# Optimization experiments

Measured on AMD Instinct MI355X. Metric: run time of the kernel, lower is better.

## Reference

```python
import math
import jax, jax.numpy as jnp
import numpy as np

N_HEAD = 8


def setup_inputs() -> dict:
    key = jax.random.key(0)
    ks = jax.random.split(key, 9)
    B, S, D = 4, 2048, 512
    s = 1.0 / math.sqrt(D)
    return {
        "x": jax.random.normal(ks[0], (B, S, D), jnp.float32),
        "Wq": jax.random.normal(ks[1], (D, D), jnp.float32) * s,
        "bq": jax.random.normal(ks[2], (D,), jnp.float32) * s,
        "Wk": jax.random.normal(ks[3], (D, D), jnp.float32) * s,
        "bk": jax.random.normal(ks[4], (D,), jnp.float32) * s,
        "Wv": jax.random.normal(ks[5], (D, D), jnp.float32) * s,
        "bv": jax.random.normal(ks[6], (D,), jnp.float32) * s,
        "Wo": jax.random.normal(ks[7], (D, D), jnp.float32) * s,
        "bo": jax.random.normal(ks[8], (D,), jnp.float32) * s,
    }


def reference(x, Wq, bq, Wk, bk, Wv, bv, Wo, bo):
    B, S, D = x.shape
    H = N_HEAD
    hd = D // H
    # projections -> [B, H, S, hd]
    def split_heads(y):
        return y.reshape(B, S, H, hd).transpose(0, 2, 1, 3)
    q = split_heads(x @ Wq + bq)
    k = split_heads(x @ Wk + bk)
    v = split_heads(x @ Wv + bv)
    scale = 1.0 / math.sqrt(hd)
    scores = jnp.einsum("bhqd,bhkd->bhqk", q, k) * scale  # [B,H,S,S]
    attn = jax.nn.softmax(scores, axis=-1)
    ctx = jnp.einsum("bhqk,bhkd->bhqd", attn, v)  # [B,H,S,hd]
    ctx = ctx.transpose(0, 2, 1, 3).reshape(B, S, D)
    out = ctx @ Wo + bo
    avg_attn = attn.mean(axis=1)  # [B,S,S]
    return out, avg_attn
```

## Files before the change

kernel.cpp:

```cpp
#include <hip/hip_runtime.h>

typedef __bf16 bf16;
typedef __bf16 bf16x8 __attribute__((ext_vector_type(8)));
typedef float  f32x4  __attribute__((ext_vector_type(4)));
typedef float  f32x16 __attribute__((ext_vector_type(16)));

#define MFMA16(a,b,c) __builtin_amdgcn_mfma_f32_16x16x32_bf16((a),(b),(c),0,0,0)
#define MFMA32(a,b,c) __builtin_amdgcn_mfma_f32_32x32x16_bf16((a),(b),(c),0,0,0)

#define BATCH 4
#define SEQ   2048
#define DIM   512
#define NH    8
#define HD    64
#define QSCALE 0.18033688f

__device__ __forceinline__ bf16x8 ldsfrag(const bf16* t, int row, int kc, int quad){
    int unit = ((kc << 2) + quad) ^ (row & 7);
    return *(const bf16x8*)(t + row * 64 + unit * 8);
}
__device__ __forceinline__ bf16x8 ldsfrag32(const bf16* t, int row, int unit){
    return *(const bf16x8*)(t + row * 64 + ((unit ^ (row & 7)) << 3));
}

__device__ __forceinline__ void stage64x64(const bf16* src, long rowStride, bf16* dst, int tid){
#pragma unroll
    for (int rnd = 0; rnd < 2; ++rnd){
        int sid = tid + rnd * 256;
        int row = sid >> 3, s = sid & 7;
        bf16x8 val = *(const bf16x8*)(src + (long)row * rowStride + s * 8);
        *(bf16x8*)(dst + row * 64 + ((s ^ (row & 7)) << 3)) = val;
    }
}

__global__ __launch_bounds__(256) void cvt_x(const float* __restrict__ x, bf16* __restrict__ xb){
    int i = blockIdx.x * 256 + threadIdx.x;
    float4 f = ((const float4*)x)[i];
    bf16* o = xb + 4 * (long)i;
    o[0] = (bf16)f.x; o[1] = (bf16)f.y; o[2] = (bf16)f.z; o[3] = (bf16)f.w;
}

__global__ __launch_bounds__(256) void cvt_wt(const float* __restrict__ Wq, const float* __restrict__ Wk,
                                              const float* __restrict__ Wv, const float* __restrict__ Wo,
                                              bf16* __restrict__ WTb){
    int z = blockIdx.z;
    const float* W = (z == 0) ? Wq : (z == 1) ? Wk : (z == 2) ? Wv : Wo;
    bf16* WT = WTb + (long)z * DIM * DIM;
    __shared__ float lt[32 * 33];
    int t = threadIdx.x, r0 = t >> 5, c = t & 31;
    int k0 = blockIdx.x * 32, n0 = blockIdx.y * 32;
#pragma unroll
    for (int i = 0; i < 4; ++i){
        int row = r0 + i * 8;
        lt[row * 33 + c] = W[(long)(k0 + row) * DIM + n0 + c];
    }
    __syncthreads();
#pragma unroll
    for (int i = 0; i < 4; ++i){
        int nr = r0 + i * 8;
        WT[(long)(n0 + nr) * DIM + k0 + c] = (bf16)lt[c * 33 + nr];
    }
}

__global__ __launch_bounds__(256) void gemm_qkv(const bf16* __restrict__ X, const bf16* __restrict__ WTb,
                                                const float* __restrict__ bq, const float* __restrict__ bk,
                                                const float* __restrict__ bv, bf16* __restrict__ outb){
    __shared__ __align__(16) bf16 lA[128 * 64];
    __shared__ __align__(16) bf16 lB[128 * 64];
    int z = blockIdx.z;
    const bf16* WT = WTb + (long)z * DIM * DIM;
    const float* bias = (z == 0) ? bq : (z == 1) ? bk : bv;
    float qs = (z == 0) ? QSCALE : 1.0f;
    bf16* out = outb + (long)z * BATCH * SEQ * DIM;
    int tid = threadIdx.x, lane = tid & 63, w = tid >> 6;
    int wm = w >> 1, wn = w & 1;
    int m0 = blockIdx.y * 128, n0 = blockIdx.x * 128;
    int r16 = lane & 15, quad = lane >> 4;
    f32x4 zz = {0.f, 0.f, 0.f, 0.f};
    f32x4 acc[4][4];
#pragma unroll
    for (int a = 0; a < 4; ++a)
#pragma unroll
        for (int b2 = 0; b2 < 4; ++b2) acc[a][b2] = zz;

    for (int k0 = 0; k0 < DIM; k0 += 64){
        __syncthreads();
#pragma unroll
        for (int rnd = 0; rnd < 4; ++rnd){
            int sid = tid + rnd * 256;
            int row = sid >> 3, s = sid & 7;
            *(bf16x8*)(lA + row * 64 + ((s ^ (row & 7)) << 3)) =
                *(const bf16x8*)(X + (long)(m0 + row) * DIM + k0 + s * 8);
            *(bf16x8*)(lB + row * 64 + ((s ^ (row & 7)) << 3)) =
                *(const bf16x8*)(WT + (long)(n0 + row) * DIM + k0 + s * 8);
        }
        __syncthreads();
#pragma unroll
        for (int kc = 0; kc < 2; ++kc){
            bf16x8 aF[4], bF[4];
#pragma unroll
            for (int i = 0; i < 4; ++i){
                aF[i] = ldsfrag(lA, wm * 64 + i * 16 + r16, kc, quad);
                bF[i] = ldsfrag(lB, wn * 64 + i * 16 + r16, kc, quad);
            }
#pragma unroll
            for (int rb = 0; rb < 4; ++rb)
#pragma unroll
                for (int nb = 0; nb < 4; ++nb)
                    acc[rb][nb] = MFMA16(aF[rb], bF[nb], acc[rb][nb]);
        }
    }
#pragma unroll
    for (int nb = 0; nb < 4; ++nb){
        int col = n0 + wn * 64 + nb * 16 + r16;
        float bv_ = bias[col];
        int hh = col >> 6, d = col & 63;
#pragma unroll
        for (int rb = 0; rb < 4; ++rb)
#pragma unroll
            for (int r = 0; r < 4; ++r){
                int row = m0 + wm * 64 + rb * 16 + quad * 4 + r;
                int bb = row >> 11, s = row & 2047;
                out[((long)(bb * NH + hh) * SEQ + s) * HD + d] = (bf16)((acc[rb][nb][r] + bv_) * qs);
            }
    }
}

__global__ __launch_bounds__(256) void vtrans(const bf16* __restrict__ v, bf16* __restrict__ vT){
    __shared__ bf16 lt[64 * 72];
    int tid = threadIdx.x;
    int s0 = blockIdx.x * 64;
    int bh = blockIdx.z * NH + blockIdx.y;
#pragma unroll
    for (int rnd = 0; rnd < 2; ++rnd){
        int sid = tid + rnd * 256;
        int row = sid >> 3, sg = sid & 7;
        *(bf16x8*)(lt + row * 72 + sg * 8) =
            *(const bf16x8*)(v + ((long)bh * SEQ + s0 + row) * HD + sg * 8);
    }
    __syncthreads();
#pragma unroll
    for (int rnd = 0; rnd < 2; ++rnd){
        int sid = tid + rnd * 256;
        int d = sid >> 3, sg = sid & 7;
        bf16x8 o;
#pragma unroll
        for (int j = 0; j < 8; ++j) o[j] = lt[(sg * 8 + j) * 72 + d];
        *(bf16x8*)(vT + ((long)bh * HD + d) * SEQ + s0 + sg * 8) = o;
    }
}

__global__ __launch_bounds__(256) void attn_flash(const bf16* __restrict__ q, const bf16* __restrict__ k,
                                                  const bf16* __restrict__ vT, bf16* __restrict__ ctx,
                                                  float* __restrict__ llv_g){
    __shared__ __align__(16) bf16 lQ[128 * 64];
    __shared__ __align__(16) bf16 lK[64 * 64];
    __shared__ __align__(16) bf16 lV[64 * 64];
    __shared__ __align__(16) bf16 lP[4][32 * 64];
    int tid = threadIdx.x, lane = tid & 63, w = tid >> 6;
    int lin = blockIdx.x + (blockIdx.y << 4) + (blockIdx.z << 7);
    int task = ((lin & 7) << 6) + (lin >> 3);
    int qt = task & 15, h = (task >> 4) & 7, b = task >> 7;
    int bh = b * NH + h;
    int q0 = qt * 128;
    int row32 = lane & 31, half = lane >> 5;
    int r3 = row32 >> 3, c7 = row32 & 7;

    {
        const bf16* src = q + ((long)bh * SEQ + q0) * HD;
#pragma unroll
        for (int rnd = 0; rnd < 4; ++rnd){
            int sid = tid + rnd * 256;
            int row = sid >> 3, s = sid & 7;
            *(bf16x8*)(lQ + row * 64 + ((s ^ (row & 7)) << 3)) =
                *(const bf16x8*)(src + (long)row * HD + s * 8);
        }
    }
    __syncthreads();
    bf16x8 qF[4];
#pragma unroll
    for (int s = 0; s < 4; ++s) qF[s] = ldsfrag32(lQ, w * 32 + row32, 2 * s + half);

    f32x16 ctxacc[2];
    float lsum[16];
#pragma unroll
    for (int i = 0; i < 16; ++i){ ctxacc[0][i] = 0.f; ctxacc[1][i] = 0.f; lsum[i] = 0.f; }

    int r0_ = tid >> 3, s_ = tid & 7;
    const bf16* kbase = k + (long)bh * SEQ * HD;
    const bf16* vbase = vT + (long)bh * HD * SEQ;
    bf16x8 kr0, kr1, vr0, vr1;
    bf16* lPw = lP[w];

    auto LOADREGS = [&](int j0){
        kr0 = *(const bf16x8*)(kbase + (long)(j0 + r0_) * HD + s_ * 8);
        kr1 = *(const bf16x8*)(kbase + (long)(j0 + r0_ + 32) * HD + s_ * 8);
        vr0 = *(const bf16x8*)(vbase + (long)r0_ * SEQ + j0 + s_ * 8);
        vr1 = *(const bf16x8*)(vbase + (long)(r0_ + 32) * SEQ + j0 + s_ * 8);
    };
    auto WRITELDS = [&](){
        int u = (s_ ^ (r0_ & 7)) << 3;
        *(bf16x8*)(lK + r0_ * 64 + u) = kr0;
        *(bf16x8*)(lK + (r0_ + 32) * 64 + u) = kr1;
        *(bf16x8*)(lV + r0_ * 64 + u) = vr0;
        *(bf16x8*)(lV + (r0_ + 32) * 64 + u) = vr1;
    };
    auto COMPUTE = [&](){
        __builtin_amdgcn_s_setprio(1);
#pragma unroll
        for (int kb = 0; kb < 2; ++kb){
            f32x16 sacc;
#pragma unroll
            for (int i = 0; i < 16; ++i) sacc[i] = 0.f;
#pragma unroll
            for (int s = 0; s < 4; ++s)
                sacc = MFMA32(qF[s], ldsfrag32(lK, kb * 32 + row32, 2 * s + half), sacc);
#pragma unroll
            for (int reg = 0; reg < 16; ++reg){
                float pp = __builtin_amdgcn_exp2f(sacc[reg]);
                lsum[reg] += pp;
                int qr = (reg & 3) + 8 * (reg >> 2) + 4 * half;
                int pu = ((kb ^ half) << 2) | (r3 ^ (reg & 3));
                lPw[qr * 64 + pu * 8 + c7] = (bf16)pp;
            }
        }
        asm volatile("s_waitcnt lgkmcnt(0)" ::: "memory");
        __builtin_amdgcn_sched_barrier(0);
        bf16x8 pF[4];
#pragma unroll
        for (int ks = 0; ks < 4; ++ks) pF[ks] = ldsfrag32(lPw, row32, 2 * ks + half);
#pragma unroll
        for (int db = 0; db < 2; ++db)
#pragma unroll
            for (int ks = 0; ks < 4; ++ks)
                ctxacc[db] = MFMA32(pF[ks], ldsfrag32(lV, db * 32 + row32, 2 * ks + half), ctxacc[db]);
        __builtin_amdgcn_s_setprio(0);
    };

    LOADREGS(0);
    WRITELDS();
    __syncthreads();
    for (int j0 = 0; j0 < SEQ - 64; j0 += 64){
        LOADREGS(j0 + 64);
        COMPUTE();
        __syncthreads();
        WRITELDS();
        __syncthreads();
    }
    COMPUTE();

#pragma unroll
    for (int m = 1; m < 32; m <<= 1)
#pragma unroll
        for (int reg = 0; reg < 16; ++reg) lsum[reg] += __shfl_xor(lsum[reg], m, 64);
    float rinv[16];
#pragma unroll
    for (int reg = 0; reg < 16; ++reg) rinv[reg] = 1.0f / lsum[reg];
#pragma unroll
    for (int db = 0; db < 2; ++db)
#pragma unroll
        for (int reg = 0; reg < 16; ++reg){
            int qr = (reg & 3) + 8 * (reg >> 2) + 4 * half;
            long srow = q0 + w * 32 + qr;
            ctx[((long)b * SEQ + srow) * DIM + h * HD + db * 32 + row32] =
                (bf16)(ctxacc[db][reg] * rinv[reg]);
        }
    if (row32 == 0)
#pragma unroll
        for (int reg = 0; reg < 16; ++reg){
            int qr = (reg & 3) + 8 * (reg >> 2) + 4 * half;
            llv_g[(long)bh * SEQ + q0 + w * 32 + qr] = -__log2f(lsum[reg]) - 3.0f;
        }
}

__global__ __launch_bounds__(256) void attn_avg(const bf16* __restrict__ q, const bf16* __restrict__ k,
                                                const float* __restrict__ llv_g, float* __restrict__ avg){
    __shared__ __align__(16) bf16 lQ[64 * 64];
    __shared__ __align__(16) bf16 lK[64 * 64];
    __shared__ __align__(16) float lsOut[4][16 * 65];
    int lin  = blockIdx.x + (blockIdx.y << 5) + (blockIdx.z << 10);
    int task = ((lin & 7) << 9) + (lin >> 3);
    int qt = task & 31;
    int jt = (task >> 5) & 31;
    int b  = task >> 10;
    int tid = threadIdx.x, lane = tid & 63, w = tid >> 6;
    int r16 = lane & 15, quad = lane >> 4;
    int qbase = qt * 64;
    int j0 = jt * 64;

    int r0_ = tid >> 3, s_ = tid & 7;
    int u_ = (s_ ^ (r0_ & 7)) << 3;
    bf16x8 qr0, qr1, kr0, kr1;
    auto LOADA = [&](int hh){
        long hA = (long)b * NH + hh;
        const bf16* qh = q + (hA * SEQ + qbase) * HD;
        const bf16* kh = k + (hA * SEQ + j0) * HD;
        qr0 = *(const bf16x8*)(qh + (long)r0_ * HD + s_ * 8);
        qr1 = *(const bf16x8*)(qh + (long)(r0_ + 32) * HD + s_ * 8);
        kr0 = *(const bf16x8*)(kh + (long)r0_ * HD + s_ * 8);
        kr1 = *(const bf16x8*)(kh + (long)(r0_ + 32) * HD + s_ * 8);
    };
    auto WRITEA = [&](){
        *(bf16x8*)(lQ + r0_ * 64 + u_) = qr0;
        *(bf16x8*)(lQ + (r0_ + 32) * 64 + u_) = qr1;
        *(bf16x8*)(lK + r0_ * 64 + u_) = kr0;
        *(bf16x8*)(lK + (r0_ + 32) * 64 + u_) = kr1;
    };

    f32x4 psum[4];
#pragma unroll
    for (int cb = 0; cb < 4; ++cb) psum[cb] = (f32x4){0.f, 0.f, 0.f, 0.f};

    LOADA(0);
    WRITEA();
    __syncthreads();
#pragma unroll 1
    for (int hh = 0; hh < NH; ++hh){
        if (hh < NH - 1) LOADA(hh + 1);
        f32x4 llv = *(const f32x4*)(llv_g + ((long)b * NH + hh) * SEQ + qbase + w * 16 + quad * 4);
        bf16x8 aF0 = ldsfrag(lQ, w * 16 + r16, 0, quad);
        bf16x8 aF1 = ldsfrag(lQ, w * 16 + r16, 1, quad);
#pragma unroll
        for (int cb = 0; cb < 4; ++cb){
            f32x4 sa = MFMA16(aF0, ldsfrag(lK, cb * 16 + r16, 0, quad), llv);
            sa = MFMA16(aF1, ldsfrag(lK, cb * 16 + r16, 1, quad), sa);
#pragma unroll
            for (int r = 0; r < 4; ++r)
                psum[cb][r] += __builtin_amdgcn_exp2f(sa[r]);
        }
        __syncthreads();
        if (hh < NH - 1){
            WRITEA();
            __syncthreads();
        }
    }

#pragma unroll
    for (int cb = 0; cb < 4; ++cb)
#pragma unroll
        for (int r = 0; r < 4; ++r)
            lsOut[w][(quad * 4 + r) * 65 + cb * 16 + r16] = psum[cb][r];
#pragma unroll
    for (int i = 0; i < 4; ++i){
        int row  = ((i >> 1) << 3) + (lane >> 3);
        int col4 = ((i & 1) << 5) + ((lane & 7) << 2);
        f32x4 v = *(const f32x4*)(&lsOut[w][row * 65 + col4]);
        __builtin_nontemporal_store(v,
            (f32x4*)&avg[((long)b * SEQ + qbase + w * 16 + row) * SEQ + j0 + col4]);
    }
}

__global__ __launch_bounds__(256) void gemm_out(const bf16* __restrict__ CTX, const bf16* __restrict__ WT,
                                                const float* __restrict__ bo, float* __restrict__ out){
    __shared__ __align__(16) bf16 lA[128 * 64];
    __shared__ __align__(16) bf16 lB[128 * 64];
    int tid = threadIdx.x, lane = tid & 63, w = tid >> 6;
    int wm = w >> 1, wn = w & 1;
    int m0 = blockIdx.y * 128, n0 = blockIdx.x * 128;
    int r16 = lane & 15, quad = lane >> 4;
    f32x4 zz = {0.f, 0.f, 0.f, 0.f};
    f32x4 acc[4][4];
#pragma unroll
    for (int a = 0; a < 4; ++a)
#pragma unroll
        for (int b2 = 0; b2 < 4; ++b2) acc[a][b2] = zz;

    for (int k0 = 0; k0 < DIM; k0 += 64){
        __syncthreads();
#pragma unroll
        for (int rnd = 0; rnd < 4; ++rnd){
            int sid = tid + rnd * 256;
            int row = sid >> 3, s = sid & 7;
            *(bf16x8*)(lA + row * 64 + ((s ^ (row & 7)) << 3)) =
                *(const bf16x8*)(CTX + (long)(m0 + row) * DIM + k0 + s * 8);
            *(bf16x8*)(lB + row * 64 + ((s ^ (row & 7)) << 3)) =
                *(const bf16x8*)(WT + (long)(n0 + row) * DIM + k0 + s * 8);
        }
        __syncthreads();
#pragma unroll
        for (int kc = 0; kc < 2; ++kc){
            bf16x8 aF[4], bF[4];
#pragma unroll
            for (int i = 0; i < 4; ++i){
                aF[i] = ldsfrag(lA, wm * 64 + i * 16 + r16, kc, quad);
                bF[i] = ldsfrag(lB, wn * 64 + i * 16 + r16, kc, quad);
            }
#pragma unroll
            for (int rb2 = 0; rb2 < 4; ++rb2)
#pragma unroll
                for (int nb = 0; nb < 4; ++nb)
                    acc[rb2][nb] = MFMA16(aF[rb2], bF[nb], acc[rb2][nb]);
        }
    }
#pragma unroll
    for (int nb = 0; nb < 4; ++nb){
        int col = n0 + wn * 64 + nb * 16 + r16;
        float bv_ = bo[col];
#pragma unroll
        for (int rb2 = 0; rb2 < 4; ++rb2)
#pragma unroll
            for (int r = 0; r < 4; ++r){
                int row = m0 + wm * 64 + rb2 * 16 + quad * 4 + r;
                out[(long)row * DIM + col] = acc[rb2][nb][r] + bv_;
            }
    }
}

extern "C" void kernel_launch(void* const* d_in, const int* in_sizes, int n_in,
                              void* d_out, int out_size, void* d_ws, size_t ws_size,
                              hipStream_t stream) {
    const float* x  = (const float*)d_in[0];
    const float* Wq = (const float*)d_in[1];
    const float* bq = (const float*)d_in[2];
    const float* Wk = (const float*)d_in[3];
    const float* bk = (const float*)d_in[4];
    const float* Wv = (const float*)d_in[5];
    const float* bv = (const float*)d_in[6];
    const float* Wo = (const float*)d_in[7];
    const float* bo = (const float*)d_in[8];
    float* out = (float*)d_out;

    char* ws = (char*)d_ws;
    bf16*  xb   = (bf16*)(ws);
    bf16*  WT   = (bf16*)(ws + 8388608);
    bf16*  qb   = (bf16*)(ws + 10485760);
    bf16*  kb   = qb + (long)BATCH * SEQ * DIM;
    bf16*  vb   = kb + (long)BATCH * SEQ * DIM;
    bf16*  vT   = (bf16*)(ws + 35651584);
    bf16*  ctx  = (bf16*)(ws + 44040192);
    float* llv  = (float*)(ws + 52428800);

    cvt_x    <<<4096, 256, 0, stream>>>(x, xb);
    cvt_wt   <<<dim3(16, 16, 4), 256, 0, stream>>>(Wq, Wk, Wv, Wo, WT);
    gemm_qkv <<<dim3(4, 64, 3), 256, 0, stream>>>(xb, WT, bq, bk, bv, qb);
    vtrans   <<<dim3(32, 8, 4), 256, 0, stream>>>(vb, vT);
    attn_flash<<<dim3(16, 8, 4), 256, 0, stream>>>(qb, kb, vT, ctx, llv);
    attn_avg <<<dim3(32, 32, 4), 256, 0, stream>>>(qb, kb, llv, out + (long)BATCH * SEQ * DIM);
    gemm_out <<<dim3(4, 64), 256, 0, stream>>>(ctx, WT + 3L * DIM * DIM, bo, out);
}
```

Baseline: 246.0 us.

## Keep attention probabilities in registers via transposed S MFMA and lane shuffles

The QK^T MFMA now takes K as the first operand, so each lane's accumulator holds a column-oriented S tile that maps onto the A-operand layout of the PV MFMA. The probabilities are packed to bf16 pairs and exchanged across the two half-waves with xor-32 shuffles, which replaces the per-wave LDS round-trip through lP and its lgkmcnt wait. Row sums collapse to one scalar per lane, so the final butterfly reduction becomes a single shuffle plus a broadcast. In exchange it adds cross-lane shuffle traffic inside the inner loop and depends on getting the MFMA fragment layout exactly right.

```diff
diff --git a/kernel.cpp b/kernel.cpp
--- a/kernel.cpp
+++ b/kernel.cpp
@@ -4,6 +4,7 @@
 typedef __bf16 bf16x8 __attribute__((ext_vector_type(8)));
 typedef float  f32x4  __attribute__((ext_vector_type(4)));
 typedef float  f32x16 __attribute__((ext_vector_type(16)));
+typedef unsigned u32x4 __attribute__((ext_vector_type(4)));
 
 #define MFMA16(a,b,c) __builtin_amdgcn_mfma_f32_16x16x32_bf16((a),(b),(c),0,0,0)
 #define MFMA32(a,b,c) __builtin_amdgcn_mfma_f32_32x32x16_bf16((a),(b),(c),0,0,0)
@@ -31,6 +32,12 @@
         bf16x8 val = *(const bf16x8*)(src + (long)row * rowStride + s * 8);
         *(bf16x8*)(dst + row * 64 + ((s ^ (row & 7)) << 3)) = val;
     }
+}
+
+__device__ __forceinline__ unsigned packbf(float lo, float hi){
+    unsigned short lb = __builtin_bit_cast(unsigned short, (bf16)lo);
+    unsigned short hb = __builtin_bit_cast(unsigned short, (bf16)hi);
+    return (unsigned)lb | ((unsigned)hb << 16);
 }
 
 __global__ __launch_bounds__(256) void cvt_x(const float* __restrict__ x, bf16* __restrict__ xb){
@@ -156,7 +163,6 @@
     __shared__ __align__(16) bf16 lQ[128 * 64];
     __shared__ __align__(16) bf16 lK[64 * 64];
     __shared__ __align__(16) bf16 lV[64 * 64];
-    __shared__ __align__(16) bf16 lP[4][32 * 64];
     int tid = threadIdx.x, lane = tid & 63, w = tid >> 6;
     int lin = blockIdx.x + (blockIdx.y << 4) + (blockIdx.z << 7);
     int task = ((lin & 7) << 6) + (lin >> 3);
@@ -164,7 +170,6 @@
     int bh = b * NH + h;
     int q0 = qt * 128;
     int row32 = lane & 31, half = lane >> 5;
-    int r3 = row32 >> 3, c7 = row32 & 7;
 
     {
         const bf16* src = q + ((long)bh * SEQ + q0) * HD;
@@ -182,15 +187,14 @@
     for (int s = 0; s < 4; ++s) qF[s] = ldsfrag32(lQ, w * 32 + row32, 2 * s + half);
 
     f32x16 ctxacc[2];
-    float lsum[16];
-#pragma unroll
-    for (int i = 0; i < 16; ++i){ ctxacc[0][i] = 0.f; ctxacc[1][i] = 0.f; lsum[i] = 0.f; }
+#pragma unroll
+    for (int i = 0; i < 16; ++i){ ctxacc[0][i] = 0.f; ctxacc[1][i] = 0.f; }
+    float lsum = 0.f;
 
     int r0_ = tid >> 3, s_ = tid & 7;
     const bf16* kbase = k + (long)bh * SEQ * HD;
     const bf16* vbase = vT + (long)bh * HD * SEQ;
     bf16x8 kr0, kr1, vr0, vr1;
-    bf16* lPw = lP[w];
 
     auto LOADREGS = [&](int j0){
         kr0 = *(const bf16x8*)(kbase + (long)(j0 + r0_) * HD + s_ * 8);
@@ -214,26 +218,39 @@
             for (int i = 0; i < 16; ++i) sacc[i] = 0.f;
 #pragma unroll
             for (int s = 0; s < 4; ++s)
-                sacc = MFMA32(qF[s], ldsfrag32(lK, kb * 32 + row32, 2 * s + half), sacc);
+                sacc = MFMA32(ldsfrag32(lK, kb * 32 + row32, 2 * s + half), qF[s], sacc);
+            float p[16];
 #pragma unroll
             for (int reg = 0; reg < 16; ++reg){
-                float pp = __builtin_amdgcn_exp2f(sacc[reg]);
-                lsum[reg] += pp;
-                int qr = (reg & 3) + 8 * (reg >> 2) + 4 * half;
-                int pu = ((kb ^ half) << 2) | (r3 ^ (reg & 3));
-                lPw[qr * 64 + pu * 8 + c7] = (bf16)pp;
-            }
-        }
-        asm volatile("s_waitcnt lgkmcnt(0)" ::: "memory");
-        __builtin_amdgcn_sched_barrier(0);
-        bf16x8 pF[4];
-#pragma unroll
-        for (int ks = 0; ks < 4; ++ks) pF[ks] = ldsfrag32(lPw, row32, 2 * ks + half);
-#pragma unroll
-        for (int db = 0; db < 2; ++db)
-#pragma unroll
-            for (int ks = 0; ks < 4; ++ks)
-                ctxacc[db] = MFMA32(pF[ks], ldsfrag32(lV, db * 32 + row32, 2 * ks + half), ctxacc[db]);
+                p[reg] = __builtin_amdgcn_exp2f(sacc[reg]);
+                lsum += p[reg];
+            }
+            unsigned Wp[4][2];
+#pragma unroll
+            for (int b2 = 0; b2 < 4; ++b2)
+#pragma unroll
+                for (int j = 0; j < 2; ++j)
+                    Wp[b2][j] = packbf(p[4 * b2 + 2 * j], p[4 * b2 + 2 * j + 1]);
+#pragma unroll
+            for (int K = 0; K < 2; ++K){
+                unsigned X0 = Wp[2 * K + 1][0], X1 = Wp[2 * K + 1][1];
+                unsigned Y0 = Wp[2 * K][0],     Y1 = Wp[2 * K][1];
+                unsigned X0p = (unsigned)__shfl_xor((int)X0, 32, 64);
+                unsigned X1p = (unsigned)__shfl_xor((int)X1, 32, 64);
+                unsigned Y0p = (unsigned)__shfl_xor((int)Y0, 32, 64);
+                unsigned Y1p = (unsigned)__shfl_xor((int)Y1, 32, 64);
+                u32x4 wv;
+                wv[0] = half ? X0p : Y0;
+                wv[1] = half ? X1p : Y1;
+                wv[2] = half ? X0  : Y0p;
+                wv[3] = half ? X1  : Y1p;
+                bf16x8 pa = __builtin_bit_cast(bf16x8, wv);
+                int ks = 2 * kb + K;
+#pragma unroll
+                for (int db = 0; db < 2; ++db)
+                    ctxacc[db] = MFMA32(pa, ldsfrag32(lV, db * 32 + row32, 2 * ks + half), ctxacc[db]);
+            }
+        }
         __builtin_amdgcn_s_setprio(0);
     };
 
@@ -249,13 +266,14 @@
     }
     COMPUTE();
 
-#pragma unroll
-    for (int m = 1; m < 32; m <<= 1)
-#pragma unroll
-        for (int reg = 0; reg < 16; ++reg) lsum[reg] += __shfl_xor(lsum[reg], m, 64);
+    lsum += __shfl_xor(lsum, 32, 64);
+    float rv = 1.0f / lsum;
     float rinv[16];
 #pragma unroll
-    for (int reg = 0; reg < 16; ++reg) rinv[reg] = 1.0f / lsum[reg];
+    for (int reg = 0; reg < 16; ++reg){
+        int qr = (reg & 3) + 8 * (reg >> 2) + 4 * half;
+        rinv[reg] = __shfl(rv, qr, 64);
+    }
 #pragma unroll
     for (int db = 0; db < 2; ++db)
 #pragma unroll
@@ -265,12 +283,8 @@
             ctx[((long)b * SEQ + srow) * DIM + h * HD + db * 32 + row32] =
                 (bf16)(ctxacc[db][reg] * rinv[reg]);
         }
-    if (row32 == 0)
-#pragma unroll
-        for (int reg = 0; reg < 16; ++reg){
-            int qr = (reg & 3) + 8 * (reg >> 2) + 4 * half;
-            llv_g[(long)bh * SEQ + q0 + w * 32 + qr] = -__log2f(lsum[reg]) - 3.0f;
-        }
+    if (half == 0)
+        llv_g[(long)bh * SEQ + q0 + w * 32 + row32] = -__log2f(lsum) - 3.0f;
 }
 
 __global__ __launch_bounds__(256) void attn_avg(const bf16* __restrict__ q, const bf16* __restrict__ k,
```

Measured after the change: 247.5 us. Within noise of the previous version (+0.6%).
